# Optimization experiments

Measured on AMD Instinct MI355X. Metric: run time of the kernel, lower is better.

## Reference

```python
import jax, jax.numpy as jnp
import numpy as np

D_MODEL = 1024
HEADS = 16
SCALE = float(np.sqrt(D_MODEL / HEADS))  # sqrt(d_k) = sqrt(64) = 8


def setup_inputs() -> dict:
    key = jax.random.key(0)
    ks = jax.random.split(key, 5)
    B, S, D = 4, 2048, D_MODEL
    q = jax.random.normal(ks[0], (B, S, D), dtype=jnp.float32)
    init = 0.02
    wq = jax.random.normal(ks[1], (D, D), dtype=jnp.float32) * init
    wk = jax.random.normal(ks[2], (D, D), dtype=jnp.float32) * init
    wv = jax.random.normal(ks[3], (D, D), dtype=jnp.float32) * init
    wo = jax.random.normal(ks[4], (D, D), dtype=jnp.float32) * init
    return {"q": q, "wq": wq, "wk": wk, "wv": wv, "wo": wo}


def reference(q, wq, wk, wv, wo):
    # Faithful to the source: NO head split is ever performed.
    B, S, D = q.shape
    # nn.Linear convention: y = x @ W.T, weight is [out, in]
    Q = jnp.einsum('bsd,ed->bse', q, wq)
    K = jnp.einsum('bsd,ed->bse', q, wk)
    V = jnp.einsum('bsd,ed->bse', q, wv)
    scores = jnp.einsum('bqe,bke->bqk', Q, K) / SCALE  # [B, S, S]
    attn = jax.nn.softmax(scores, axis=-1)
    out = jnp.einsum('bqk,bke->bqe', attn, V)  # [B, S, D]
    # Source bug reproduced: transpose(1,2).contiguous().view(B, S, -1)
    # => reshape the [B, D, S] contiguous buffer back to [B, S, D].
    out = jnp.transpose(out, (0, 2, 1)).reshape(B, S, D)
    return jnp.einsum('bsd,ed->bse', out, wo)
```

## Files before the change

kernel.cpp:

```cpp
#include <hip/hip_runtime.h>
#include <hip/hip_bf16.h>
#include <stdint.h>

typedef __bf16 bf16;
typedef __attribute__((ext_vector_type(8))) __bf16 bf16x8;
typedef __attribute__((ext_vector_type(4))) float f32x4;
typedef __attribute__((ext_vector_type(8))) unsigned short u16x8;

#define LDS_U32 __attribute__((address_space(3))) uint32_t
#define GLB_U32 const __attribute__((address_space(1))) uint32_t
#define GLOAD16(g, l) __builtin_amdgcn_global_load_lds((GLB_U32*)(g), (LDS_U32*)(l), 16, 0, 0)

#define DSR(dst, addr, OFFLIT) \
  asm volatile("ds_read_b128 %0, %1 offset:" OFFLIT : "=v"(dst) : "v"(addr))

#define WAIT_LGKM0() asm volatile("s_waitcnt lgkmcnt(0)")
#define WAIT_LGKM4() asm volatile("s_waitcnt lgkmcnt(4)")
#define WAIT_VMN(n)  asm volatile("s_waitcnt vmcnt(" #n ")")
#define SB()         __builtin_amdgcn_sched_barrier(0)

__global__ __launch_bounds__(256) void cvt_all(const float* __restrict__ q,
                                               const float* __restrict__ wq,
                                               const float* __restrict__ wk,
                                               const float* __restrict__ wv,
                                               const float* __restrict__ wo,
                                               bf16* __restrict__ qb,
                                               bf16* __restrict__ W3,
                                               bf16* __restrict__ wob) {
  const int b = blockIdx.x;
  const float* src;
  bf16* dst;
  int within;
  if (b < 2048) { src = q; dst = qb; within = b; }
  else {
    const int seg = (b - 2048) >> 8;
    within = (b - 2048) & 255;
    if (seg == 0)      { src = wq; dst = W3; }
    else if (seg == 1) { src = wk; dst = W3 + 1048576; }
    else if (seg == 2) { src = wv; dst = W3 + 2097152; }
    else               { src = wo; dst = wob; }
  }
  const int off = within * 1024;
#pragma unroll
  for (int it = 0; it < 4; ++it) {
    const int j = off + it * 256 + threadIdx.x;
    float4 v = reinterpret_cast<const float4*>(src)[j];
    ushort4 o;
    o.x = __builtin_bit_cast(unsigned short, (bf16)v.x);
    o.y = __builtin_bit_cast(unsigned short, (bf16)v.y);
    o.z = __builtin_bit_cast(unsigned short, (bf16)v.z);
    o.w = __builtin_bit_cast(unsigned short, (bf16)v.w);
    reinterpret_cast<ushort4*>(dst)[j] = o;
  }
}

template <int EPI, int WN>
__global__ __launch_bounds__(512, 2) void g256(const bf16* __restrict__ A,
                                               const bf16* __restrict__ Bm,
                                               void* __restrict__ Cp,
                                               int K, float alpha,
                                               long sA, long sB, long sC, int ldc,
                                               int CW, int CH) {
  constexpr int BN = WN * 64;
  constexpr uint32_t PARB = 32768u + WN * 8192u;
  __shared__ bf16 smem_[PARB];
  const long z = blockIdx.z;
  const int t = threadIdx.x;
  const int l = t & 63;
  const int w = t >> 6;
  const int wr = (w >> 2) * 128;
  const int wc = (w & 3) * (WN * 16);
  const int NT = K >> 6;

  int bx, by;
  {
    const int gx = (int)gridDim.x;
    const int gy = (int)gridDim.y;
    const int nxy = gx * gy;
    const int f = (int)blockIdx.y * gx + (int)blockIdx.x;
    const int cgx = (CW > 0) ? gx / CW : 0;
    if ((nxy & 7) == 0 && CW > 0 && CH > 0 && gx % CW == 0 && gy % CH == 0 &&
        cgx * (gy / CH) == 8) {
      const int xcd = f & 7;
      const int i = f >> 3;
      const int cx = xcd % cgx;
      const int cy = xcd / cgx;
      bx = cx * CW + (i % CW);
      by = cy * CH + (i / CW);
    } else if ((nxy & 7) == 0) {
      const int qq = nxy >> 3;
      const int wg = (f & 7) * qq + (f >> 3);
      bx = wg % gx;
      by = wg / gx;
    } else {
      bx = (int)blockIdx.x;
      by = (int)blockIdx.y;
    }
  }

  const bf16* Ab = A + z * sA + (long)(by * 256) * K;
  const bf16* Bb = Bm + z * sB + (long)(bx * BN) * K;

  uint32_t loc = (uint32_t)t * 16u;
  uint32_t g0 = loc ^ (((loc >> 9) & 1u) << 5);
  const int r0 = (int)(((g0 >> 10) >> 1) * 16 + ((g0 >> 6) & 15));
  const int c0 = (int)(((g0 >> 10) & 1) * 32 + ((g0 & 63) >> 1));

  uint32_t lo_ = (uint32_t)((l & 15) * 64 + (l >> 4) * 16);
  const uint32_t lane_off = lo_ ^ (((lo_ >> 9) & 1u) << 5);
  const uint32_t aRegion = (uint32_t)(wr >> 7) * 16384u;
  const uint32_t smem_base = (uint32_t)(size_t)&smem_[0];
  const uint32_t aBase = smem_base + aRegion + lane_off;

  uint32_t bA[WN];
#pragma unroll
  for (int n = 0; n < WN; ++n) {
    const uint32_t row = (uint32_t)(wc + n * 16);
    bA[n] = smem_base + 32768u + (row >> 6) * 8192u + ((row & 63u) >> 4) * 2048u + lane_off;
  }

  auto STAGE1 = [&](const bf16* mat, int unit, int tile, uint32_t isB) {
    uint32_t dst = (uint32_t)(tile & 1) * PARB + isB + (uint32_t)unit * 8192u + (uint32_t)t * 16u;
    const bf16* src = mat + (long)(unit * 64 + r0) * K + tile * 64 + c0;
    GLOAD16(src, smem_ + (dst >> 1));
  };

  f32x4 acc[8][WN] = {};

  STAGE1(Ab, 0, 0, 0u); STAGE1(Ab, 1, 0, 0u); STAGE1(Ab, 2, 0, 0u); STAGE1(Ab, 3, 0, 0u);
#pragma unroll
  for (int u = 0; u < WN; ++u) STAGE1(Bb, u, 0, 32768u);
  SB();
  WAIT_VMN(0);
  __builtin_amdgcn_s_barrier();

#define MFMAQ(Q, S)                                                                  \
  _Pragma("unroll") for (int mi = 0; mi < 2; ++mi)                                   \
  _Pragma("unroll") for (int n = 0; n < WN; ++n)                                     \
  _Pragma("unroll") for (int kk = 0; kk < 2; ++kk)                                   \
    acc[(Q) * 2 + mi][n] = __builtin_amdgcn_mfma_f32_16x16x32_bf16(                  \
        __builtin_bit_cast(bf16x8, aF[S][mi][kk]), __builtin_bit_cast(bf16x8, bF[n][kk]), \
        acc[(Q) * 2 + mi][n], 0, 0, 0);

  for (int T = 0; T < NT; ++T) {
    const uint32_t pb = (uint32_t)(T & 1) * PARB;
    const uint32_t aA = aBase + pb;
    f32x4 bF[WN][2];
    f32x4 aF[2][2][2];

    if (T + 1 < NT) {
#pragma unroll
      for (int u = 0; u < WN; ++u) STAGE1(Bb, u, T + 1, 32768u);
      STAGE1(Ab, 0, T + 1, 0u); STAGE1(Ab, 2, T + 1, 0u);
    }

#pragma unroll
    for (int n = 0; n < WN; ++n) {
      DSR(bF[n][0], bA[n] + pb, "0");
      DSR(bF[n][1], bA[n] + pb, "1024");
    }
    DSR(aF[0][0][0], aA, "0");    DSR(aF[0][0][1], aA, "1024");
    DSR(aF[0][1][0], aA, "2048"); DSR(aF[0][1][1], aA, "3072");
    DSR(aF[1][0][0], aA, "4096"); DSR(aF[1][0][1], aA, "5120");
    DSR(aF[1][1][0], aA, "6144"); DSR(aF[1][1][1], aA, "7168");
    WAIT_LGKM4();
    SB();
    __builtin_amdgcn_s_setprio(1);
    MFMAQ(0, 0)
    __builtin_amdgcn_s_setprio(0);
    WAIT_LGKM0();
    SB();
    __builtin_amdgcn_s_setprio(1);
    MFMAQ(1, 1)
    __builtin_amdgcn_s_setprio(0);

    if (T + 1 < NT) { STAGE1(Ab, 1, T + 1, 0u); STAGE1(Ab, 3, T + 1, 0u); }

    SB();
    if (T + 1 < NT) {
      if constexpr (WN == 2) { WAIT_VMN(6); } else { WAIT_VMN(8); }
    } else {
      WAIT_VMN(0);
    }
    __builtin_amdgcn_s_barrier();

    DSR(aF[0][0][0], aA, "8192");  DSR(aF[0][0][1], aA, "9216");
    DSR(aF[0][1][0], aA, "10240"); DSR(aF[0][1][1], aA, "11264");
    DSR(aF[1][0][0], aA, "12288"); DSR(aF[1][0][1], aA, "13312");
    DSR(aF[1][1][0], aA, "14336"); DSR(aF[1][1][1], aA, "15360");
    WAIT_LGKM4();
    SB();
    __builtin_amdgcn_s_setprio(1);
    MFMAQ(2, 0)
    __builtin_amdgcn_s_setprio(0);
    WAIT_LGKM0();
    SB();
    __builtin_amdgcn_s_setprio(1);
    MFMAQ(3, 1)
    __builtin_amdgcn_s_setprio(0);

    SB();
    if (T + 1 < NT) { WAIT_VMN(2); } else { WAIT_VMN(0); }
    __builtin_amdgcn_s_barrier();
  }
#undef MFMAQ

  if constexpr (EPI == 4) {
    constexpr int STR = 264;
#pragma unroll
    for (int m = 0; m < 8; ++m)
#pragma unroll
      for (int n = 0; n < WN; ++n) {
        const int e = wc + n * 16 + (l & 15);
        const int s = wr + (l >> 4) * 4 + m * 16;
        ushort4 pk;
        pk.x = __builtin_bit_cast(unsigned short, (bf16)(acc[m][n][0] * alpha));
        pk.y = __builtin_bit_cast(unsigned short, (bf16)(acc[m][n][1] * alpha));
        pk.z = __builtin_bit_cast(unsigned short, (bf16)(acc[m][n][2] * alpha));
        pk.w = __builtin_bit_cast(unsigned short, (bf16)(acc[m][n][3] * alpha));
        *reinterpret_cast<ushort4*>(&smem_[e * STR + s]) = pk;
      }
    __syncthreads();
    bf16* Vt = (bf16*)Cp;
    const int bq = by >> 3;
    const int sbase = (by & 7) * 256;
    const int e0 = t >> 2;
#pragma unroll
    for (int it = 0; it < 8; ++it) {
      const int c = (t & 3) + it * 4;
      uint4 v = *reinterpret_cast<const uint4*>(&smem_[e0 * STR + c * 8]);
      *reinterpret_cast<uint4*>(
          &Vt[(long)bq * 2097152 + (long)(bx * BN + e0) * 2048 + sbase + c * 8]) = v;
    }
    return;
  }

  const int orow0 = by * 256 + wr + (l >> 4) * 4;
  const int ocol0 = bx * BN + wc + (l & 15);
#pragma unroll
  for (int m = 0; m < 8; ++m)
#pragma unroll
    for (int n = 0; n < WN; ++n)
#pragma unroll
      for (int i = 0; i < 4; ++i) {
        const long r = orow0 + m * 16 + i;
        const long c = ocol0 + n * 16;
        const float v = acc[m][n][i] * alpha;
        if constexpr (EPI == 0) {
          ((bf16*)Cp)[z * sC + r * ldc + c] = (bf16)v;
        } else if constexpr (EPI == 2) {
          ((float*)Cp)[r * ldc + c] = v;
        } else if constexpr (EPI == 5) {
          bf16* Qb = (bf16*)Cp;
          bf16* Kb = Qb + 8388608;
          if (c < 1024) Qb[r * 1024 + c] = (bf16)v;
          else Kb[r * 1024 + (c - 1024)] = (bf16)v;
        }
      }
}

__global__ __launch_bounds__(256) void softmax_rows(bf16* __restrict__ P) {
  const long row = blockIdx.x;
  bf16* p = P + row * 2048;
  const int t = threadIdx.x;
  const int lane = t & 63;
  const int wave = t >> 6;

  u16x8 raw = *reinterpret_cast<const u16x8*>(p + t * 8);
  float v[8];
#pragma unroll
  for (int j = 0; j < 8; ++j) {
    uint32_t bits = ((uint32_t)raw[j]) << 16;
    v[j] = __builtin_bit_cast(float, bits);
  }
  float m = v[0];
#pragma unroll
  for (int j = 1; j < 8; ++j) m = fmaxf(m, v[j]);
#pragma unroll
  for (int off = 32; off > 0; off >>= 1) m = fmaxf(m, __shfl_xor(m, off, 64));
  __shared__ float redm[4];
  __shared__ float reds[4];
  if (lane == 0) redm[wave] = m;
  __syncthreads();
  m = fmaxf(fmaxf(redm[0], redm[1]), fmaxf(redm[2], redm[3]));

  float s = 0.f;
#pragma unroll
  for (int j = 0; j < 8; ++j) {
    v[j] = __expf(v[j] - m);
    s += v[j];
  }
#pragma unroll
  for (int off = 32; off > 0; off >>= 1) s += __shfl_xor(s, off, 64);
  if (lane == 0) reds[wave] = s;
  __syncthreads();
  s = reds[0] + reds[1] + reds[2] + reds[3];
  const float inv = 1.f / s;

  u16x8 o;
#pragma unroll
  for (int j = 0; j < 8; ++j) o[j] = __builtin_bit_cast(unsigned short, (bf16)(v[j] * inv));
  *reinterpret_cast<u16x8*>(p + t * 8) = o;
}

extern "C" void kernel_launch(void* const* d_in, const int* in_sizes, int n_in,
                              void* d_out, int out_size, void* d_ws, size_t ws_size,
                              hipStream_t stream) {
  const float* q = (const float*)d_in[0];
  const float* wq = (const float*)d_in[1];
  const float* wk = (const float*)d_in[2];
  const float* wv = (const float*)d_in[3];
  const float* wo = (const float*)d_in[4];
  float* out = (float*)d_out;

  constexpr int B = 4, S = 2048, D = 1024;
  constexpr long SD = (long)S * D;
  constexpr long SS = (long)S * S;
  constexpr long DD = (long)D * D;

  bf16* wsb = (bf16*)d_ws;
  bf16* qb = wsb;
  bf16* W3 = qb + B * SD;
  bf16* wob = W3 + 3 * DD;
  bf16* Qb = wob + DD;
  bf16* Kb = Qb + B * SD;
  bf16* Vt = Kb + B * SD;
  bf16* P = Vt + B * SD;
  bf16* X = P + B * SS;

  cvt_all<<<3072, 256, 0, stream>>>(q, wq, wk, wv, wo, qb, W3, wob);

  g256<5, 4><<<dim3(8, 32, 1), 512, 0, stream>>>(qb, W3, Qb, D, 1.f, 0, 0, 0, 0, 4, 8);
  g256<4, 2><<<dim3(8, 32, 1), 512, 0, stream>>>(qb, W3 + 2 * DD, Vt, D, 1.f, 0, 0, 0, 0, 4, 8);
  g256<0, 4><<<dim3(8, 8, B), 512, 0, stream>>>(Qb, Kb, P, D, 0.125f, SD, SD, SS, S, 4, 2);
  softmax_rows<<<B * S, 256, 0, stream>>>(P);
  g256<0, 2><<<dim3(16, 4, B), 512, 0, stream>>>(Vt, P, X, S, 1.f, SD, SS, SD, S, 4, 2);
  g256<2, 2><<<dim3(8, 32, 1), 512, 0, stream>>>(X, wob, out, D, 1.f, 0, 0, 0, D, 4, 8);
}
```

Before: 185.1 us.

## Fuse V projection into the Q/K projection GEMM kernel

The Q/K projection kernel now runs a second K-loop after storing Q and K. That loop reuses the same A tiles (the bf16 input rows) against a 128-column slice of the V weight and writes V transposed through LDS. This removes one kernel launch and the separate V projection kernel's reload of the input rows. In exchange, each block does serial extra work with a different tile shape (WN=2 on 128 columns), and the A tiles are still restaged from global memory in the second loop.

```diff
diff --git a/kernel.cpp b/kernel.cpp
--- a/kernel.cpp
+++ b/kernel.cpp
@@ -235,6 +235,129 @@
     return;
   }
 
+  if constexpr (EPI == 6) {
+    {
+      const int orow0 = by * 256 + wr + (l >> 4) * 4;
+      const int ocol0 = bx * 256 + wc + (l & 15);
+      bf16* Qb = (bf16*)Cp;
+      bf16* Kb = Qb + 8388608;
+#pragma unroll
+      for (int m = 0; m < 8; ++m)
+#pragma unroll
+        for (int n = 0; n < WN; ++n)
+#pragma unroll
+          for (int i = 0; i < 4; ++i) {
+            const long r = orow0 + m * 16 + i;
+            const long c = ocol0 + n * 16;
+            const float v = acc[m][n][i];
+            if (c < 1024) Qb[r * 1024 + c] = (bf16)v;
+            else Kb[r * 1024 + (c - 1024)] = (bf16)v;
+          }
+    }
+    const bf16* Bv = Bm + 2 * 1048576 + (long)(bx * 128) * K;
+    uint32_t bA2[2];
+#pragma unroll
+    for (int n = 0; n < 2; ++n) {
+      const uint32_t row = (uint32_t)((w & 3) * 32 + n * 16);
+      bA2[n] = smem_base + 32768u + (row >> 6) * 8192u + ((row & 63u) >> 4) * 2048u + lane_off;
+    }
+#pragma unroll
+    for (int m = 0; m < 8; ++m)
+#pragma unroll
+      for (int n = 0; n < 2; ++n) acc[m][n] = f32x4{0.f, 0.f, 0.f, 0.f};
+
+    __builtin_amdgcn_s_barrier();
+    STAGE1(Ab, 0, 0, 0u); STAGE1(Ab, 1, 0, 0u); STAGE1(Ab, 2, 0, 0u); STAGE1(Ab, 3, 0, 0u);
+    STAGE1(Bv, 0, 0, 32768u); STAGE1(Bv, 1, 0, 32768u);
+    SB();
+    WAIT_VMN(0);
+    __builtin_amdgcn_s_barrier();
+
+#define MFMAQ2(Q, S)                                                                 \
+    _Pragma("unroll") for (int mi = 0; mi < 2; ++mi)                                 \
+    _Pragma("unroll") for (int n = 0; n < 2; ++n)                                    \
+    _Pragma("unroll") for (int kk = 0; kk < 2; ++kk)                                 \
+      acc[(Q) * 2 + mi][n] = __builtin_amdgcn_mfma_f32_16x16x32_bf16(                \
+          __builtin_bit_cast(bf16x8, aF[S][mi][kk]), __builtin_bit_cast(bf16x8, bF2[n][kk]), \
+          acc[(Q) * 2 + mi][n], 0, 0, 0);
+
+    for (int T = 0; T < NT; ++T) {
+      const uint32_t pb = (uint32_t)(T & 1) * PARB;
+      const uint32_t aA = aBase + pb;
+      f32x4 bF2[2][2];
+      f32x4 aF[2][2][2];
+      if (T + 1 < NT) {
+        STAGE1(Ab, 0, T + 1, 0u); STAGE1(Ab, 1, T + 1, 0u);
+        STAGE1(Ab, 2, T + 1, 0u); STAGE1(Ab, 3, T + 1, 0u);
+        STAGE1(Bv, 0, T + 1, 32768u); STAGE1(Bv, 1, T + 1, 32768u);
+      }
+      DSR(bF2[0][0], bA2[0] + pb, "0"); DSR(bF2[0][1], bA2[0] + pb, "1024");
+      DSR(bF2[1][0], bA2[1] + pb, "0"); DSR(bF2[1][1], bA2[1] + pb, "1024");
+      DSR(aF[0][0][0], aA, "0");    DSR(aF[0][0][1], aA, "1024");
+      DSR(aF[0][1][0], aA, "2048"); DSR(aF[0][1][1], aA, "3072");
+      DSR(aF[1][0][0], aA, "4096"); DSR(aF[1][0][1], aA, "5120");
+      DSR(aF[1][1][0], aA, "6144"); DSR(aF[1][1][1], aA, "7168");
+      WAIT_LGKM4();
+      SB();
+      __builtin_amdgcn_s_setprio(1);
+      MFMAQ2(0, 0)
+      __builtin_amdgcn_s_setprio(0);
+      WAIT_LGKM0();
+      SB();
+      __builtin_amdgcn_s_setprio(1);
+      MFMAQ2(1, 1)
+      __builtin_amdgcn_s_setprio(0);
+      DSR(aF[0][0][0], aA, "8192");  DSR(aF[0][0][1], aA, "9216");
+      DSR(aF[0][1][0], aA, "10240"); DSR(aF[0][1][1], aA, "11264");
+      DSR(aF[1][0][0], aA, "12288"); DSR(aF[1][0][1], aA, "13312");
+      DSR(aF[1][1][0], aA, "14336"); DSR(aF[1][1][1], aA, "15360");
+      WAIT_LGKM4();
+      SB();
+      __builtin_amdgcn_s_setprio(1);
+      MFMAQ2(2, 0)
+      __builtin_amdgcn_s_setprio(0);
+      WAIT_LGKM0();
+      SB();
+      __builtin_amdgcn_s_setprio(1);
+      MFMAQ2(3, 1)
+      __builtin_amdgcn_s_setprio(0);
+      SB();
+      if (T + 1 < NT) { WAIT_VMN(0); } else { WAIT_VMN(0); }
+      __builtin_amdgcn_s_barrier();
+    }
+#undef MFMAQ2
+
+    {
+      constexpr int STR = 264;
+#pragma unroll
+      for (int m = 0; m < 8; ++m)
+#pragma unroll
+        for (int n = 0; n < 2; ++n) {
+          const int e = (w & 3) * 32 + n * 16 + (l & 15);
+          const int s = wr + (l >> 4) * 4 + m * 16;
+          ushort4 pk;
+          pk.x = __builtin_bit_cast(unsigned short, (bf16)acc[m][n][0]);
+          pk.y = __builtin_bit_cast(unsigned short, (bf16)acc[m][n][1]);
+          pk.z = __builtin_bit_cast(unsigned short, (bf16)acc[m][n][2]);
+          pk.w = __builtin_bit_cast(unsigned short, (bf16)acc[m][n][3]);
+          *reinterpret_cast<ushort4*>(&smem_[e * STR + s]) = pk;
+        }
+      __syncthreads();
+      bf16* Vt = (bf16*)Cp + 2 * 8388608;
+      const int bq = by >> 3;
+      const int sbase = (by & 7) * 256;
+      const int e0 = t >> 2;
+#pragma unroll
+      for (int it = 0; it < 8; ++it) {
+        const int c = (t & 3) + it * 4;
+        uint4 v = *reinterpret_cast<const uint4*>(&smem_[e0 * STR + c * 8]);
+        *reinterpret_cast<uint4*>(
+            &Vt[(long)bq * 2097152 + (long)(bx * 128 + e0) * 2048 + sbase + c * 8]) = v;
+      }
+    }
+    return;
+  }
+
   const int orow0 = by * 256 + wr + (l >> 4) * 4;
   const int ocol0 = bx * BN + wc + (l & 15);
 #pragma unroll
@@ -250,11 +373,6 @@
           ((bf16*)Cp)[z * sC + r * ldc + c] = (bf16)v;
         } else if constexpr (EPI == 2) {
           ((float*)Cp)[r * ldc + c] = v;
-        } else if constexpr (EPI == 5) {
-          bf16* Qb = (bf16*)Cp;
-          bf16* Kb = Qb + 8388608;
-          if (c < 1024) Qb[r * 1024 + c] = (bf16)v;
-          else Kb[r * 1024 + (c - 1024)] = (bf16)v;
         }
       }
 }
@@ -330,8 +448,7 @@
 
   cvt_all<<<3072, 256, 0, stream>>>(q, wq, wk, wv, wo, qb, W3, wob);
 
-  g256<5, 4><<<dim3(8, 32, 1), 512, 0, stream>>>(qb, W3, Qb, D, 1.f, 0, 0, 0, 0, 4, 8);
-  g256<4, 2><<<dim3(8, 32, 1), 512, 0, stream>>>(qb, W3 + 2 * DD, Vt, D, 1.f, 0, 0, 0, 0, 4, 8);
+  g256<6, 4><<<dim3(8, 32, 1), 512, 0, stream>>>(qb, W3, Qb, D, 1.f, 0, 0, 0, 0, 4, 8);
   g256<0, 4><<<dim3(8, 8, B), 512, 0, stream>>>(Qb, Kb, P, D, 0.125f, SD, SD, SS, S, 4, 2);
   softmax_rows<<<B * S, 256, 0, stream>>>(P);
   g256<0, 2><<<dim3(16, 4, B), 512, 0, stream>>>(Vt, P, X, S, 1.f, SD, SS, SD, S, 4, 2);
```

Result: faster. 181.2 us (-2.1%).
